# Kernel tuning notes

Measured on AMD Instinct MI355X. Metric: run time of the kernel, lower is better.

Reference implementation:

```python
import jax, jax.numpy as jnp
import numpy as np

DIM = 1024
N_HEADS = 16
B, S = 2, 2048


def setup_inputs() -> dict:
    key = jax.random.key(0)
    ks = jax.random.split(key, 9)
    scale = 1.0 / np.sqrt(DIM)
    return {
        "i1": jax.random.normal(ks[0], (B, S, DIM), jnp.float32),
        "i2": jax.random.normal(ks[1], (B, S, DIM), jnp.float32),
        "cr": jax.random.normal(ks[2], (B, S, 2), jnp.float32),
        # Linear params stored as [in, out] so forward is x @ W + b (same math as torch x W^T + b)
        "Wq": jax.random.normal(ks[3], (DIM, DIM), jnp.float32) * scale,
        "bq": jnp.zeros((DIM,), jnp.float32),
        "Wkv": jax.random.normal(ks[4], (DIM, 2 * DIM), jnp.float32) * scale,
        "bkv": jnp.zeros((2 * DIM,), jnp.float32),
        "Wmo": jax.random.normal(ks[5], (2, DIM), jnp.float32) * (1.0 / np.sqrt(2.0)),
        "bmo": jnp.zeros((DIM,), jnp.float32),
    }


def reference(i1, i2, cr, Wq, bq, Wkv, bkv, Wmo, bmo):
    H = N_HEADS
    Dh = DIM // H
    b, s, _ = i1.shape

    q = (i1 @ Wq + bq).reshape(b, s, H, Dh)                # [B,S,H,Dh]
    kv = i2 @ Wkv + bkv                                     # [B,S,2*DIM]
    k = kv[..., :DIM].reshape(b, s, H, Dh)
    v = kv[..., DIM:].reshape(b, s, H, Dh)
    mo = (cr @ Wmo + bmo).reshape(b, s, H, Dh)              # [B,S,H,Dh]

    scores = jnp.einsum("bqhd,bkhd->bhqk", q, k) / jnp.sqrt(jnp.asarray(Dh, q.dtype))
    probs = jax.nn.softmax(scores, axis=-1)                 # [B,H,S,S] (dropout p=0)

    h = jnp.einsum("bhqk,bkhd->bqhd", probs, v).reshape(b, s, DIM)
    m = jnp.einsum("bhqk,bkhd->bqhd", probs, mo).reshape(b, s, DIM)
    return h, m
```

## Files before the change

kernel.cpp:

```cpp
#include <hip/hip_runtime.h>
#include <hip/hip_bf16.h>

typedef __attribute__((ext_vector_type(8))) short short8;
typedef __attribute__((ext_vector_type(4))) short short4_t;
typedef __attribute__((ext_vector_type(4))) float f32x4;
typedef unsigned short ushort_t;

#define DEV __device__ __forceinline__

DEV ushort_t f2bf(float f) {
    unsigned u = __builtin_bit_cast(unsigned, f);
    u = u + 0x7fffu + ((u >> 16) & 1u);
    return (ushort_t)(u >> 16);
}

DEV unsigned pk_bf16(float lo, float hi) {
    __hip_bfloat162 h = __float22bfloat162_rn(make_float2(lo, hi));
    unsigned u;
    __builtin_memcpy(&u, &h, sizeof(u));
    return u;
}

DEV float fast_exp2(float x) {
#if __has_builtin(__builtin_amdgcn_exp2f)
    return __builtin_amdgcn_exp2f(x);
#else
    float r;
    asm("v_exp_f32 %0, %1" : "=v"(r) : "v"(x));
    return r;
#endif
}

DEV short8 ld8(const ushort_t* p) { return *reinterpret_cast<const short8*>(p); }

__global__ __launch_bounds__(256)
void cvt_bf16(const float* __restrict__ in, ushort_t* __restrict__ out)
{
    const size_t i = ((size_t)blockIdx.x * 256 + threadIdx.x) * 8;
    const float4 a = *reinterpret_cast<const float4*>(in + i);
    const float4 b = *reinterpret_cast<const float4*>(in + i + 4);
    short8 v;
    v[0] = (short)f2bf(a.x); v[1] = (short)f2bf(a.y);
    v[2] = (short)f2bf(a.z); v[3] = (short)f2bf(a.w);
    v[4] = (short)f2bf(b.x); v[5] = (short)f2bf(b.y);
    v[6] = (short)f2bf(b.z); v[7] = (short)f2bf(b.w);
    *reinterpret_cast<short8*>(out + i) = v;
}

__global__ __launch_bounds__(256)
void tcvt_bf16(const float* __restrict__ W, ushort_t* __restrict__ Wt, int K, int N)
{
    __shared__ ushort_t tile[64][72];
    const int t = threadIdx.x;
    const int nx = blockIdx.x * 64, ky = blockIdx.y * 64;
    const int r = t >> 2, q = (t & 3) * 16;

    const float* src = W + (size_t)(ky + r) * N + nx + q;
#pragma unroll
    for (int i = 0; i < 4; ++i) {
        const float4 v = *reinterpret_cast<const float4*>(src + 4 * i);
        tile[r][q + 4 * i + 0] = f2bf(v.x);
        tile[r][q + 4 * i + 1] = f2bf(v.y);
        tile[r][q + 4 * i + 2] = f2bf(v.z);
        tile[r][q + 4 * i + 3] = f2bf(v.w);
    }
    __syncthreads();
    short8 o0, o1;
#pragma unroll
    for (int i = 0; i < 8; ++i) {
        o0[i] = (short)tile[q + i][r];
        o1[i] = (short)tile[q + 8 + i][r];
    }
    ushort_t* dst = Wt + (size_t)(nx + r) * K + ky + q;
    *reinterpret_cast<short8*>(dst) = o0;
    *reinterpret_cast<short8*>(dst + 8) = o1;
}

__global__ __launch_bounds__(256, 2)
void proj_all(const ushort_t* __restrict__ A1, const ushort_t* __restrict__ A2,
              const ushort_t* __restrict__ Wqt, const ushort_t* __restrict__ Wkvt,
              const float* __restrict__ bqv, const float* __restrict__ bkv,
              ushort_t* __restrict__ Qr, ushort_t* __restrict__ Kr,
              ushort_t* __restrict__ Vt)
{
    __shared__ ushort_t As[128 * 72];
    __shared__ ushort_t Bs[128 * 72];

    const int t = threadIdx.x;
    const int lane = t & 63;
    const int wv = t >> 6;
    const int wr = wv >> 1, wc = wv & 1;
    const int c = lane & 15, g = lane >> 4;
    const int m0 = blockIdx.y * 128;
    const int nblk = blockIdx.x;

    const ushort_t* A;
    const ushort_t* Wt;
    const float* bias;
    int n0;
    if (nblk < 8) { A = A1; Wt = Wqt;  bias = bqv; n0 = nblk * 128; }
    else          { A = A2; Wt = Wkvt; bias = bkv; n0 = (nblk - 8) * 128; }
    const bool isQ = (nblk < 8);

    f32x4 acc[4][4];
    const f32x4 zero4 = {0.f, 0.f, 0.f, 0.f};
#pragma unroll
    for (int mi = 0; mi < 4; ++mi)
#pragma unroll
        for (int ni = 0; ni < 4; ++ni) acc[mi][ni] = zero4;

    const int srow[4] = { (t + 0)   >> 3, (t + 256) >> 3, (t + 512) >> 3, (t + 768) >> 3 };
    const int skq     = (t & 7) * 8;

    short8 a_reg[4], b_reg[4];
#pragma unroll
    for (int rep = 0; rep < 4; ++rep) {
        a_reg[rep] = ld8(A  + (size_t)(m0 + srow[rep]) * 1024 + skq);
        b_reg[rep] = ld8(Wt + (size_t)(n0 + srow[rep]) * 1024 + skq);
    }

    for (int it = 0; it < 16; ++it) {
#pragma unroll
        for (int rep = 0; rep < 4; ++rep) {
            *reinterpret_cast<short8*>(&As[srow[rep] * 72 + skq]) = a_reg[rep];
            *reinterpret_cast<short8*>(&Bs[srow[rep] * 72 + skq]) = b_reg[rep];
        }
        __syncthreads();
        if (it < 15) {
            const int k1 = (it + 1) * 64;
#pragma unroll
            for (int rep = 0; rep < 4; ++rep) {
                a_reg[rep] = ld8(A  + (size_t)(m0 + srow[rep]) * 1024 + k1 + skq);
                b_reg[rep] = ld8(Wt + (size_t)(n0 + srow[rep]) * 1024 + k1 + skq);
            }
        }
#pragma unroll
        for (int kk = 0; kk < 64; kk += 32) {
            short8 afr[4], bfr[4];
#pragma unroll
            for (int mi = 0; mi < 4; ++mi)
                afr[mi] = ld8(&As[(wr * 64 + mi * 16 + c) * 72 + kk + 8 * g]);
#pragma unroll
            for (int ni = 0; ni < 4; ++ni)
                bfr[ni] = ld8(&Bs[(wc * 64 + ni * 16 + c) * 72 + kk + 8 * g]);
#pragma unroll
            for (int mi = 0; mi < 4; ++mi)
#pragma unroll
                for (int ni = 0; ni < 4; ++ni)
                    acc[mi][ni] = __builtin_amdgcn_mfma_f32_16x16x32_bf16(
                        afr[mi], bfr[ni], acc[mi][ni], 0, 0, 0);
        }
        __syncthreads();
    }

#pragma unroll
    for (int mi = 0; mi < 4; ++mi) {
#pragma unroll
        for (int ni = 0; ni < 4; ++ni) {
            const int n = n0 + wc * 64 + ni * 16 + c;
            const float bb = bias[n];
#pragma unroll
            for (int j = 0; j < 4; ++j) {
                const int m = m0 + wr * 64 + mi * 16 + 4 * g + j;
                const int b = m >> 11, s = m & 2047;
                const ushort_t val = f2bf(acc[mi][ni][j] + bb);
                if (isQ) {
                    Qr[((size_t)((b * 16 + (n >> 6)) * 2048 + s)) * 64 + (n & 63)] = val;
                } else if (n < 1024) {
                    Kr[((size_t)((b * 16 + (n >> 6)) * 2048 + s)) * 64 + (n & 63)] = val;
                } else {
                    const int np = n - 1024;
                    Vt[(size_t)((b * 16 + (np >> 6)) * 64 + (np & 63)) * 2048 + s] = val;
                }
            }
        }
    }
}

__global__ __launch_bounds__(256)
void proj_gemm(const float* __restrict__ A, const float* __restrict__ W,
               const float* __restrict__ bias, int N,
               ushort_t* __restrict__ outRow, ushort_t* __restrict__ outT)
{
    __shared__ ushort_t As[128 * 72];
    __shared__ ushort_t Bt[128 * 72];

    const int t = threadIdx.x;
    const int lane = t & 63;
    const int wv = t >> 6;
    const int wr = wv >> 1, wc = wv & 1;
    const int c = lane & 15, g = lane >> 4;
    const int m0 = blockIdx.y * 128, n0 = blockIdx.x * 128;

    f32x4 acc[4][4];
    const f32x4 zero4 = {0.f, 0.f, 0.f, 0.f};
#pragma unroll
    for (int mi = 0; mi < 4; ++mi)
#pragma unroll
        for (int ni = 0; ni < 4; ++ni) acc[mi][ni] = zero4;

    for (int it = 0; it < 16; ++it) {
        const int k0 = it * 64;
        {
            const int kq = (t & 15) * 4;
            int r = t >> 4;
#pragma unroll
            for (int rep = 0; rep < 8; ++rep, r += 16) {
                float4 v = *reinterpret_cast<const float4*>(
                    A + (size_t)(m0 + r) * 1024 + k0 + kq);
                ushort_t* dst = &As[r * 72 + kq];
                dst[0] = f2bf(v.x); dst[1] = f2bf(v.y);
                dst[2] = f2bf(v.z); dst[3] = f2bf(v.w);
            }
        }
        {
            const int nq = (t & 31) * 4;
            const int kr = t >> 5;
#pragma unroll
            for (int rep = 0; rep < 8; ++rep) {
                const int k = kr + 8 * rep;
                float4 v = *reinterpret_cast<const float4*>(
                    W + (size_t)(k0 + k) * N + n0 + nq);
                Bt[(nq + 0) * 72 + k] = f2bf(v.x);
                Bt[(nq + 1) * 72 + k] = f2bf(v.y);
                Bt[(nq + 2) * 72 + k] = f2bf(v.z);
                Bt[(nq + 3) * 72 + k] = f2bf(v.w);
            }
        }
        __syncthreads();
#pragma unroll
        for (int kk = 0; kk < 64; kk += 32) {
            short8 afr[4], bfr[4];
#pragma unroll
            for (int mi = 0; mi < 4; ++mi)
                afr[mi] = ld8(&As[(wr * 64 + mi * 16 + c) * 72 + kk + 8 * g]);
#pragma unroll
            for (int ni = 0; ni < 4; ++ni)
                bfr[ni] = ld8(&Bt[(wc * 64 + ni * 16 + c) * 72 + kk + 8 * g]);
#pragma unroll
            for (int mi = 0; mi < 4; ++mi)
#pragma unroll
                for (int ni = 0; ni < 4; ++ni)
                    acc[mi][ni] = __builtin_amdgcn_mfma_f32_16x16x32_bf16(
                        afr[mi], bfr[ni], acc[mi][ni], 0, 0, 0);
        }
        __syncthreads();
    }

#pragma unroll
    for (int mi = 0; mi < 4; ++mi) {
#pragma unroll
        for (int ni = 0; ni < 4; ++ni) {
            const int n = n0 + wc * 64 + ni * 16 + c;
            const float bb = bias[n];
#pragma unroll
            for (int j = 0; j < 4; ++j) {
                const int m = m0 + wr * 64 + mi * 16 + 4 * g + j;
                const int b = m >> 11, s = m & 2047;
                const ushort_t val = f2bf(acc[mi][ni][j] + bb);
                if (outT != nullptr && n >= 1024) {
                    const int np = n - 1024;
                    const int hh = np >> 6, d = np & 63;
                    outT[(size_t)((b * 16 + hh) * 64 + d) * 2048 + s] = val;
                } else {
                    const int hh = n >> 6, d = n & 63;
                    outRow[((size_t)((b * 16 + hh) * 2048 + s)) * 64 + d] = val;
                }
            }
        }
    }
}

DEV void tile_compute(const ushort_t* __restrict__ Ks, const ushort_t* __restrict__ Vs,
                      const float* __restrict__ Crs, int c, int g,
                      const short8 (&bq)[2][2],
                      f32x4 (&accv)[2][4], float (&lst)[2],
                      float (&a0s)[2], float (&a1s)[2])
{
    const f32x4 zero4 = {0.f, 0.f, 0.f, 0.f};
    const float SCL = 0.18033688011112042f;
    const int kxor = (c & 7) << 3;
    const int vxor = (c & 7) << 2;

    short8 KC[2][2];
#pragma unroll
    for (int ct = 0; ct < 2; ++ct)
#pragma unroll
        for (int st = 0; st < 2; ++st)
            KC[ct][st] = ld8(&Ks[(ct * 16 + c) * 64 + ((st * 32 + 8 * g) ^ kxor)]);
    short8 VC[4];
#pragma unroll
    for (int dt = 0; dt < 4; ++dt) {
        const short4_t vlo = *reinterpret_cast<const short4_t*>(
            &Vs[(dt * 16 + c) * 32 + ((4 * g) ^ vxor)]);
        const short4_t vhi = *reinterpret_cast<const short4_t*>(
            &Vs[(dt * 16 + c) * 32 + ((4 * g + 16) ^ vxor)]);
        VC[dt] = __builtin_shufflevector(vlo, vhi, 0, 1, 2, 3, 4, 5, 6, 7);
    }
    float4 cc[2][2];
#pragma unroll
    for (int ct = 0; ct < 2; ++ct) {
        const float4* cp = reinterpret_cast<const float4*>(Crs + (16 * ct + 4 * g) * 2);
        cc[ct][0] = cp[0];
        cc[ct][1] = cp[1];
    }

    f32x4 sc[2][2];
#pragma unroll
    for (int qt = 0; qt < 2; ++qt)
#pragma unroll
        for (int ct = 0; ct < 2; ++ct) {
            f32x4 z = zero4;
            z = __builtin_amdgcn_mfma_f32_16x16x32_bf16(KC[ct][0], bq[qt][0], z, 0, 0, 0);
            z = __builtin_amdgcn_mfma_f32_16x16x32_bf16(KC[ct][1], bq[qt][1], z, 0, 0, 0);
            sc[qt][ct] = z;
        }

    short8 pa[2];
#pragma unroll
    for (int qt = 0; qt < 2; ++qt) {
        float e[2][4];
        float lc = lst[qt], a0c = a0s[qt], a1c = a1s[qt];
#pragma unroll
        for (int ct = 0; ct < 2; ++ct) {
            const float cr0[4] = {cc[ct][0].x, cc[ct][0].z, cc[ct][1].x, cc[ct][1].z};
            const float cr1[4] = {cc[ct][0].y, cc[ct][0].w, cc[ct][1].y, cc[ct][1].w};
#pragma unroll
            for (int j = 0; j < 4; ++j) {
                const float ev = fast_exp2(sc[qt][ct][j] * SCL);
                e[ct][j] = ev;
                lc  += ev;
                a0c += ev * cr0[j];
                a1c += ev * cr1[j];
            }
        }
        lst[qt] = lc; a0s[qt] = a0c; a1s[qt] = a1c;
        int4 w;
        w.x = (int)pk_bf16(e[0][0], e[0][1]);
        w.y = (int)pk_bf16(e[0][2], e[0][3]);
        w.z = (int)pk_bf16(e[1][0], e[1][1]);
        w.w = (int)pk_bf16(e[1][2], e[1][3]);
        pa[qt] = __builtin_bit_cast(short8, w);
    }

#pragma unroll
    for (int dt = 0; dt < 4; ++dt) {
        accv[0][dt] = __builtin_amdgcn_mfma_f32_16x16x32_bf16(VC[dt], pa[0], accv[0][dt], 0, 0, 0);
        accv[1][dt] = __builtin_amdgcn_mfma_f32_16x16x32_bf16(VC[dt], pa[1], accv[1][dt], 0, 0, 0);
    }
}

DEV void pair_body(const ushort_t* __restrict__ Kh, const ushort_t* __restrict__ Vh,
                   const float* __restrict__ crb, int kvA, int kvB,
                   const ushort_t* KsC0, const ushort_t* VsC0, const float* CrC0,
                   const ushort_t* KsC1, const ushort_t* VsC1, const float* CrC1,
                   ushort_t* KsN0, ushort_t* VsN0, float* CrN0,
                   ushort_t* KsN1, ushort_t* VsN1, float* CrN1,
                   int t, int c, int g, int rk, int ck, int rv, int cv,
                   int kaddr, int vaddr0, int vaddr1,
                   const short8 (&bq)[2][2],
                   f32x4 (&accv)[2][4], float (&lst)[2],
                   float (&a0s)[2], float (&a1s)[2])
{
    const short8 kregA = ld8(Kh + (size_t)(kvA + rk) * 64 + ck);
    const short8 vregA = ld8(Vh + (size_t)rv * 2048 + kvA + cv);
    const short8 kregB = ld8(Kh + (size_t)(kvB + rk) * 64 + ck);
    const short8 vregB = ld8(Vh + (size_t)rv * 2048 + kvB + cv);
    float2 crreg = make_float2(0.f, 0.f);
    if (t < 64) {
        const int kvX = (t & 32) ? kvB : kvA;
        crreg = *reinterpret_cast<const float2*>(crb + (size_t)(kvX + (t & 31)) * 2);
    }
    __builtin_amdgcn_sched_barrier(0);

    tile_compute(KsC0, VsC0, CrC0, c, g, bq, accv, lst, a0s, a1s);
    tile_compute(KsC1, VsC1, CrC1, c, g, bq, accv, lst, a0s, a1s);

    *reinterpret_cast<short8*>(&KsN0[kaddr]) = kregA;
    *reinterpret_cast<short8*>(&KsN1[kaddr]) = kregB;
    *reinterpret_cast<short4_t*>(&VsN0[vaddr0]) = __builtin_shufflevector(vregA, vregA, 0, 1, 2, 3);
    *reinterpret_cast<short4_t*>(&VsN0[vaddr1]) = __builtin_shufflevector(vregA, vregA, 4, 5, 6, 7);
    *reinterpret_cast<short4_t*>(&VsN1[vaddr0]) = __builtin_shufflevector(vregB, vregB, 0, 1, 2, 3);
    *reinterpret_cast<short4_t*>(&VsN1[vaddr1]) = __builtin_shufflevector(vregB, vregB, 4, 5, 6, 7);
    if (t < 64) {
        float* d = (t & 32) ? CrN1 : CrN0;
        *reinterpret_cast<float2*>(d + (t & 31) * 2) = crreg;
    }
    __syncthreads();
}

__global__ __launch_bounds__(256, 2)
void attn_kernel(const ushort_t* __restrict__ Qr, const ushort_t* __restrict__ Kr,
                 const ushort_t* __restrict__ Vt, const float* __restrict__ cr,
                 const float* __restrict__ Wmo, const float* __restrict__ bmo,
                 float* __restrict__ out)
{
    __shared__ ushort_t smem[16896];
    ushort_t* K0 = smem;            ushort_t* K1 = smem + 2048;
    ushort_t* K2 = smem + 4096;     ushort_t* K3 = smem + 6144;
    ushort_t* V0 = smem + 8192;     ushort_t* V1 = smem + 10240;
    ushort_t* V2 = smem + 12288;    ushort_t* V3 = smem + 14336;
    float* C0 = reinterpret_cast<float*>(smem + 16384);
    float* C1 = C0 + 64;  float* C2 = C0 + 128;  float* C3 = C0 + 192;

    const int t = threadIdx.x;
    const int w = t >> 6, lane = t & 63;
    const int c = lane & 15, g = lane >> 4;
    const int rk = t >> 3, ck = (t & 7) * 8;
    const int rv = t >> 2, cv = (t & 3) * 8;
    const int kaddr  = rk * 64 + (ck ^ ((rk & 7) << 3));
    const int vaddr0 = rv * 32 + (cv ^ ((rv & 7) << 2));
    const int vaddr1 = rv * 32 + ((cv + 4) ^ ((rv & 7) << 2));

    const int gid = blockIdx.x;
    const int bh = (gid & 7) + 8 * ((gid >> 3) & 3);
    const int xt = gid >> 5;
    const int b = bh >> 4, hh = bh & 15;
    const int qb = xt * 128 + w * 32;

    const ushort_t* Qh = Qr + (size_t)bh * (2048 * 64);
    const ushort_t* Kh = Kr + (size_t)bh * (2048 * 64);
    const ushort_t* Vh = Vt + (size_t)bh * (64 * 2048);
    const float*   crb = cr + (size_t)b * (2048 * 2);

    short8 bq[2][2];
#pragma unroll
    for (int qt = 0; qt < 2; ++qt)
#pragma unroll
        for (int st = 0; st < 2; ++st)
            bq[qt][st] = ld8(Qh + (size_t)(qb + qt * 16 + c) * 64 + st * 32 + 8 * g);

    f32x4 accv[2][4];
    const f32x4 zero4 = {0.f, 0.f, 0.f, 0.f};
#pragma unroll
    for (int qt = 0; qt < 2; ++qt)
#pragma unroll
        for (int dt = 0; dt < 4; ++dt) accv[qt][dt] = zero4;

    float lst[2] = {0.f, 0.f};
    float a0s[2] = {0.f, 0.f};
    float a1s[2] = {0.f, 0.f};

    {
        const short8 kA = ld8(Kh + (size_t)rk * 64 + ck);
        const short8 vA = ld8(Vh + (size_t)rv * 2048 + cv);
        const short8 kB = ld8(Kh + (size_t)(32 + rk) * 64 + ck);
        const short8 vB = ld8(Vh + (size_t)rv * 2048 + 32 + cv);
        *reinterpret_cast<short8*>(&K0[kaddr]) = kA;
        *reinterpret_cast<short8*>(&K1[kaddr]) = kB;
        *reinterpret_cast<short4_t*>(&V0[vaddr0]) = __builtin_shufflevector(vA, vA, 0, 1, 2, 3);
        *reinterpret_cast<short4_t*>(&V0[vaddr1]) = __builtin_shufflevector(vA, vA, 4, 5, 6, 7);
        *reinterpret_cast<short4_t*>(&V1[vaddr0]) = __builtin_shufflevector(vB, vB, 0, 1, 2, 3);
        *reinterpret_cast<short4_t*>(&V1[vaddr1]) = __builtin_shufflevector(vB, vB, 4, 5, 6, 7);
        if (t < 64) {
            const int kvX = (t & 32) ? 32 : 0;
            const float2 v = *reinterpret_cast<const float2*>(crb + (size_t)(kvX + (t & 31)) * 2);
            float* d = (t & 32) ? C1 : C0;
            *reinterpret_cast<float2*>(d + (t & 31) * 2) = v;
        }
    }
    __syncthreads();

    for (int i = 0; i < 16; ++i) {
        const int base = i * 128;
        pair_body(Kh, Vh, crb, base + 64, base + 96,
                  K0, V0, C0, K1, V1, C1,
                  K2, V2, C2, K3, V3, C3,
                  t, c, g, rk, ck, rv, cv, kaddr, vaddr0, vaddr1,
                  bq, accv, lst, a0s, a1s);
        pair_body(Kh, Vh, crb, (base + 128) & 2047, (base + 160) & 2047,
                  K2, V2, C2, K3, V3, C3,
                  K0, V0, C0, K1, V1, C1,
                  t, c, g, rk, ck, rv, cv, kaddr, vaddr0, vaddr1,
                  bq, accv, lst, a0s, a1s);
    }

#pragma unroll
    for (int qt = 0; qt < 2; ++qt) {
        lst[qt] += __shfl_xor(lst[qt], 16, 64); lst[qt] += __shfl_xor(lst[qt], 32, 64);
        a0s[qt] += __shfl_xor(a0s[qt], 16, 64); a0s[qt] += __shfl_xor(a0s[qt], 32, 64);
        a1s[qt] += __shfl_xor(a1s[qt], 16, 64); a1s[qt] += __shfl_xor(a1s[qt], 32, 64);
    }

#pragma unroll
    for (int qt = 0; qt < 2; ++qt) {
        const int q = qb + qt * 16 + c;
        const float inv = 1.f / lst[qt];
        const float a0 = a0s[qt] * inv, a1 = a1s[qt] * inv;
#pragma unroll
        for (int dt = 0; dt < 4; ++dt) {
            const int d = hh * 64 + dt * 16 + 4 * g;
            const float4 w0 = *reinterpret_cast<const float4*>(Wmo + d);
            const float4 w1 = *reinterpret_cast<const float4*>(Wmo + 1024 + d);
            const float4 bm = *reinterpret_cast<const float4*>(bmo + d);
            const size_t oidx = ((size_t)(b * 2048 + q)) * 1024 + d;
            float4 hv, mv;
            hv.x = accv[qt][dt][0] * inv; hv.y = accv[qt][dt][1] * inv;
            hv.z = accv[qt][dt][2] * inv; hv.w = accv[qt][dt][3] * inv;
            mv.x = a0 * w0.x + a1 * w1.x + bm.x;
            mv.y = a0 * w0.y + a1 * w1.y + bm.y;
            mv.z = a0 * w0.z + a1 * w1.z + bm.z;
            mv.w = a0 * w0.w + a1 * w1.w + bm.w;
            *reinterpret_cast<float4*>(out + oidx) = hv;
            *reinterpret_cast<float4*>(out + 4194304 + oidx) = mv;
        }
    }
}

extern "C" void kernel_launch(void* const* d_in, const int* in_sizes, int n_in,
                              void* d_out, int out_size, void* d_ws, size_t ws_size,
                              hipStream_t stream)
{
    const float* i1  = (const float*)d_in[0];
    const float* i2  = (const float*)d_in[1];
    const float* cr  = (const float*)d_in[2];
    const float* Wq  = (const float*)d_in[3];
    const float* bq  = (const float*)d_in[4];
    const float* Wkv = (const float*)d_in[5];
    const float* bkv = (const float*)d_in[6];
    const float* Wmo = (const float*)d_in[7];
    const float* bmo = (const float*)d_in[8];
    float* out = (float*)d_out;

    ushort_t* Qr = (ushort_t*)d_ws;
    ushort_t* Kr = Qr + 4194304;
    ushort_t* Vt = Kr + 4194304;

    if (ws_size >= 48234496ULL) {
        ushort_t* A1   = Vt + 4194304;
        ushort_t* A2   = A1 + 4194304;
        ushort_t* Wqt  = A2 + 4194304;
        ushort_t* Wkvt = Wqt + 1048576;
        cvt_bf16<<<dim3(2048), dim3(256), 0, stream>>>(i1, A1);
        cvt_bf16<<<dim3(2048), dim3(256), 0, stream>>>(i2, A2);
        tcvt_bf16<<<dim3(16, 16), dim3(256), 0, stream>>>(Wq, Wqt, 1024, 1024);
        tcvt_bf16<<<dim3(32, 16), dim3(256), 0, stream>>>(Wkv, Wkvt, 1024, 2048);
        proj_all<<<dim3(24, 32), dim3(256), 0, stream>>>(A1, A2, Wqt, Wkvt, bq, bkv, Qr, Kr, Vt);
    } else {
        proj_gemm<<<dim3(8, 32), dim3(256), 0, stream>>>(i1, Wq, bq, 1024, Qr, nullptr);
        proj_gemm<<<dim3(16, 32), dim3(256), 0, stream>>>(i2, Wkv, bkv, 2048, Kr, Vt);
    }
    attn_kernel<<<dim3(512), dim3(256), 0, stream>>>(Qr, Kr, Vt, cr, Wmo, bmo, out);
}
```

Before: 122.2 us.

## Compute softmax row-sum and cr moments via MFMA, fold scale into Q projection

The per-element VALU accumulation of the softmax denominator and the two cr-weighted sums is replaced by an extra MFMA per q-tile. It multiplies a small bf16 stats tile (a row of ones, two rows of cr values, zero padding) against the probability fragments. The softmax scale is also folded into the Q projection epilogue, which removes a multiply before each exp2. This moves VALU work onto the matrix cores, at the cost of bf16 rounding of cr values and of Q after scaling, plus a little extra shared memory.

```diff
diff --git a/kernel.cpp b/kernel.cpp
--- a/kernel.cpp
+++ b/kernel.cpp
@@ -32,6 +32,8 @@
 }
 
 DEV short8 ld8(const ushort_t* p) { return *reinterpret_cast<const short8*>(p); }
+
+#define SCL_F 0.18033688011112042f
 
 __global__ __launch_bounds__(256)
 void cvt_bf16(const float* __restrict__ in, ushort_t* __restrict__ out)
@@ -101,6 +103,7 @@
     if (nblk < 8) { A = A1; Wt = Wqt;  bias = bqv; n0 = nblk * 128; }
     else          { A = A2; Wt = Wkvt; bias = bkv; n0 = (nblk - 8) * 128; }
     const bool isQ = (nblk < 8);
+    const float qscale = isQ ? SCL_F : 1.0f;
 
     f32x4 acc[4][4];
     const f32x4 zero4 = {0.f, 0.f, 0.f, 0.f};
@@ -163,7 +166,7 @@
             for (int j = 0; j < 4; ++j) {
                 const int m = m0 + wr * 64 + mi * 16 + 4 * g + j;
                 const int b = m >> 11, s = m & 2047;
-                const ushort_t val = f2bf(acc[mi][ni][j] + bb);
+                const ushort_t val = f2bf((acc[mi][ni][j] + bb) * qscale);
                 if (isQ) {
                     Qr[((size_t)((b * 16 + (n >> 6)) * 2048 + s)) * 64 + (n & 63)] = val;
                 } else if (n < 1024) {
@@ -191,6 +194,7 @@
     const int wr = wv >> 1, wc = wv & 1;
     const int c = lane & 15, g = lane >> 4;
     const int m0 = blockIdx.y * 128, n0 = blockIdx.x * 128;
+    const float qscale = (outT == nullptr) ? SCL_F : 1.0f;
 
     f32x4 acc[4][4];
     const f32x4 zero4 = {0.f, 0.f, 0.f, 0.f};
@@ -257,7 +261,7 @@
             for (int j = 0; j < 4; ++j) {
                 const int m = m0 + wr * 64 + mi * 16 + 4 * g + j;
                 const int b = m >> 11, s = m & 2047;
-                const ushort_t val = f2bf(acc[mi][ni][j] + bb);
+                const ushort_t val = f2bf((acc[mi][ni][j] + bb) * qscale);
                 if (outT != nullptr && n >= 1024) {
                     const int np = n - 1024;
                     const int hh = np >> 6, d = np & 63;
@@ -272,13 +276,11 @@
 }
 
 DEV void tile_compute(const ushort_t* __restrict__ Ks, const ushort_t* __restrict__ Vs,
-                      const float* __restrict__ Crs, int c, int g,
+                      const ushort_t* __restrict__ Sts, int c, int g,
                       const short8 (&bq)[2][2],
-                      f32x4 (&accv)[2][4], float (&lst)[2],
-                      float (&a0s)[2], float (&a1s)[2])
+                      f32x4 (&accv)[2][4], f32x4 (&stat)[2])
 {
     const f32x4 zero4 = {0.f, 0.f, 0.f, 0.f};
-    const float SCL = 0.18033688011112042f;
     const int kxor = (c & 7) << 3;
     const int vxor = (c & 7) << 2;
 
@@ -297,13 +299,11 @@
             &Vs[(dt * 16 + c) * 32 + ((4 * g + 16) ^ vxor)]);
         VC[dt] = __builtin_shufflevector(vlo, vhi, 0, 1, 2, 3, 4, 5, 6, 7);
     }
-    float4 cc[2][2];
-#pragma unroll
-    for (int ct = 0; ct < 2; ++ct) {
-        const float4* cp = reinterpret_cast<const float4*>(Crs + (16 * ct + 4 * g) * 2);
-        cc[ct][0] = cp[0];
-        cc[ct][1] = cp[1];
-    }
+    const short4_t slo = *reinterpret_cast<const short4_t*>(
+        &Sts[c * 32 + ((4 * g) ^ vxor)]);
+    const short4_t shi = *reinterpret_cast<const short4_t*>(
+        &Sts[c * 32 + ((4 * g + 16) ^ vxor)]);
+    const short8 stf = __builtin_shufflevector(slo, shi, 0, 1, 2, 3, 4, 5, 6, 7);
 
     f32x4 sc[2][2];
 #pragma unroll
@@ -320,21 +320,11 @@
 #pragma unroll
     for (int qt = 0; qt < 2; ++qt) {
         float e[2][4];
-        float lc = lst[qt], a0c = a0s[qt], a1c = a1s[qt];
-#pragma unroll
-        for (int ct = 0; ct < 2; ++ct) {
-            const float cr0[4] = {cc[ct][0].x, cc[ct][0].z, cc[ct][1].x, cc[ct][1].z};
-            const float cr1[4] = {cc[ct][0].y, cc[ct][0].w, cc[ct][1].y, cc[ct][1].w};
-#pragma unroll
-            for (int j = 0; j < 4; ++j) {
-                const float ev = fast_exp2(sc[qt][ct][j] * SCL);
-                e[ct][j] = ev;
-                lc  += ev;
-                a0c += ev * cr0[j];
-                a1c += ev * cr1[j];
-            }
-        }
-        lst[qt] = lc; a0s[qt] = a0c; a1s[qt] = a1c;
+#pragma unroll
+        for (int ct = 0; ct < 2; ++ct)
+#pragma unroll
+            for (int j = 0; j < 4; ++j)
+                e[ct][j] = fast_exp2(sc[qt][ct][j]);
         int4 w;
         w.x = (int)pk_bf16(e[0][0], e[0][1]);
         w.y = (int)pk_bf16(e[0][2], e[0][3]);
@@ -344,6 +334,9 @@
     }
 
 #pragma unroll
+    for (int qt = 0; qt < 2; ++qt)
+        stat[qt] = __builtin_amdgcn_mfma_f32_16x16x32_bf16(stf, pa[qt], stat[qt], 0, 0, 0);
+#pragma unroll
     for (int dt = 0; dt < 4; ++dt) {
         accv[0][dt] = __builtin_amdgcn_mfma_f32_16x16x32_bf16(VC[dt], pa[0], accv[0][dt], 0, 0, 0);
         accv[1][dt] = __builtin_amdgcn_mfma_f32_16x16x32_bf16(VC[dt], pa[1], accv[1][dt], 0, 0, 0);
@@ -352,29 +345,31 @@
 
 DEV void pair_body(const ushort_t* __restrict__ Kh, const ushort_t* __restrict__ Vh,
                    const float* __restrict__ crb, int kvA, int kvB,
-                   const ushort_t* KsC0, const ushort_t* VsC0, const float* CrC0,
-                   const ushort_t* KsC1, const ushort_t* VsC1, const float* CrC1,
-                   ushort_t* KsN0, ushort_t* VsN0, float* CrN0,
-                   ushort_t* KsN1, ushort_t* VsN1, float* CrN1,
+                   const ushort_t* KsC0, const ushort_t* VsC0, const ushort_t* StC0,
+                   const ushort_t* KsC1, const ushort_t* VsC1, const ushort_t* StC1,
+                   ushort_t* KsN0, ushort_t* VsN0, ushort_t* StN0,
+                   ushort_t* KsN1, ushort_t* VsN1, ushort_t* StN1,
                    int t, int c, int g, int rk, int ck, int rv, int cv,
                    int kaddr, int vaddr0, int vaddr1,
                    const short8 (&bq)[2][2],
-                   f32x4 (&accv)[2][4], float (&lst)[2],
-                   float (&a0s)[2], float (&a1s)[2])
+                   f32x4 (&accv)[2][4], f32x4 (&stat)[2])
 {
     const short8 kregA = ld8(Kh + (size_t)(kvA + rk) * 64 + ck);
     const short8 vregA = ld8(Vh + (size_t)rv * 2048 + kvA + cv);
     const short8 kregB = ld8(Kh + (size_t)(kvB + rk) * 64 + ck);
     const short8 vregB = ld8(Vh + (size_t)rv * 2048 + kvB + cv);
-    float2 crreg = make_float2(0.f, 0.f);
-    if (t < 64) {
-        const int kvX = (t & 32) ? kvB : kvA;
-        crreg = *reinterpret_cast<const float2*>(crb + (size_t)(kvX + (t & 31)) * 2);
+    ushort_t crsh = 0; int staddr = 0;
+    if (t < 128) {
+        const int kvX = (t & 64) ? kvB : kvA;
+        const int row = 1 + ((t >> 5) & 1);
+        const float v = crb[(size_t)(kvX + (t & 31)) * 2 + (row - 1)];
+        crsh = f2bf(v);
+        staddr = row * 32 + ((t & 31) ^ ((row & 7) << 2));
     }
     __builtin_amdgcn_sched_barrier(0);
 
-    tile_compute(KsC0, VsC0, CrC0, c, g, bq, accv, lst, a0s, a1s);
-    tile_compute(KsC1, VsC1, CrC1, c, g, bq, accv, lst, a0s, a1s);
+    tile_compute(KsC0, VsC0, StC0, c, g, bq, accv, stat);
+    tile_compute(KsC1, VsC1, StC1, c, g, bq, accv, stat);
 
     *reinterpret_cast<short8*>(&KsN0[kaddr]) = kregA;
     *reinterpret_cast<short8*>(&KsN1[kaddr]) = kregB;
@@ -382,10 +377,7 @@
     *reinterpret_cast<short4_t*>(&VsN0[vaddr1]) = __builtin_shufflevector(vregA, vregA, 4, 5, 6, 7);
     *reinterpret_cast<short4_t*>(&VsN1[vaddr0]) = __builtin_shufflevector(vregB, vregB, 0, 1, 2, 3);
     *reinterpret_cast<short4_t*>(&VsN1[vaddr1]) = __builtin_shufflevector(vregB, vregB, 4, 5, 6, 7);
-    if (t < 64) {
-        float* d = (t & 32) ? CrN1 : CrN0;
-        *reinterpret_cast<float2*>(d + (t & 31) * 2) = crreg;
-    }
+    if (t < 128) ((t & 64) ? StN1 : StN0)[staddr] = crsh;
     __syncthreads();
 }
 
@@ -395,13 +387,13 @@
                  const float* __restrict__ Wmo, const float* __restrict__ bmo,
                  float* __restrict__ out)
 {
-    __shared__ ushort_t smem[16896];
+    __shared__ ushort_t smem[18432];
     ushort_t* K0 = smem;            ushort_t* K1 = smem + 2048;
     ushort_t* K2 = smem + 4096;     ushort_t* K3 = smem + 6144;
     ushort_t* V0 = smem + 8192;     ushort_t* V1 = smem + 10240;
     ushort_t* V2 = smem + 12288;    ushort_t* V3 = smem + 14336;
-    float* C0 = reinterpret_cast<float*>(smem + 16384);
-    float* C1 = C0 + 64;  float* C2 = C0 + 128;  float* C3 = C0 + 192;
+    ushort_t* S0 = smem + 16384;    ushort_t* S1 = smem + 16896;
+    ushort_t* S2 = smem + 17408;    ushort_t* S3 = smem + 17920;
 
     const int t = threadIdx.x;
     const int w = t >> 6, lane = t & 63;
@@ -431,15 +423,20 @@
             bq[qt][st] = ld8(Qh + (size_t)(qb + qt * 16 + c) * 64 + st * 32 + 8 * g);
 
     f32x4 accv[2][4];
+    f32x4 stat[2];
     const f32x4 zero4 = {0.f, 0.f, 0.f, 0.f};
 #pragma unroll
-    for (int qt = 0; qt < 2; ++qt)
+    for (int qt = 0; qt < 2; ++qt) {
+        stat[qt] = zero4;
 #pragma unroll
         for (int dt = 0; dt < 4; ++dt) accv[qt][dt] = zero4;
-
-    float lst[2] = {0.f, 0.f};
-    float a0s[2] = {0.f, 0.f};
-    float a1s[2] = {0.f, 0.f};
+    }
+
+    for (int idx = t; idx < 2048; idx += 256) {
+        const int row = (idx >> 5) & 15;
+        if (row != 1 && row != 2)
+            smem[16384 + idx] = (row == 0) ? (ushort_t)0x3F80 : (ushort_t)0;
+    }
 
     {
         const short8 kA = ld8(Kh + (size_t)rk * 64 + ck);
@@ -452,11 +449,11 @@
         *reinterpret_cast<short4_t*>(&V0[vaddr1]) = __builtin_shufflevector(vA, vA, 4, 5, 6, 7);
         *reinterpret_cast<short4_t*>(&V1[vaddr0]) = __builtin_shufflevector(vB, vB, 0, 1, 2, 3);
         *reinterpret_cast<short4_t*>(&V1[vaddr1]) = __builtin_shufflevector(vB, vB, 4, 5, 6, 7);
-        if (t < 64) {
-            const int kvX = (t & 32) ? 32 : 0;
-            const float2 v = *reinterpret_cast<const float2*>(crb + (size_t)(kvX + (t & 31)) * 2);
-            float* d = (t & 32) ? C1 : C0;
-            *reinterpret_cast<float2*>(d + (t & 31) * 2) = v;
+        if (t < 128) {
+            const int kvX = (t & 64) ? 32 : 0;
+            const int row = 1 + ((t >> 5) & 1);
+            const float v = crb[(size_t)(kvX + (t & 31)) * 2 + (row - 1)];
+            ((t & 64) ? S1 : S0)[row * 32 + ((t & 31) ^ ((row & 7) << 2))] = f2bf(v);
         }
     }
     __syncthreads();
@@ -464,22 +461,23 @@
     for (int i = 0; i < 16; ++i) {
         const int base = i * 128;
         pair_body(Kh, Vh, crb, base + 64, base + 96,
-                  K0, V0, C0, K1, V1, C1,
-                  K2, V2, C2, K3, V3, C3,
+                  K0, V0, S0, K1, V1, S1,
+                  K2, V2, S2, K3, V3, S3,
                   t, c, g, rk, ck, rv, cv, kaddr, vaddr0, vaddr1,
-                  bq, accv, lst, a0s, a1s);
+                  bq, accv, stat);
         pair_body(Kh, Vh, crb, (base + 128) & 2047, (base + 160) & 2047,
-                  K2, V2, C2, K3, V3, C3,
-                  K0, V0, C0, K1, V1, C1,
+                  K2, V2, S2, K3, V3, S3,
+                  K0, V0, S0, K1, V1, S1,
                   t, c, g, rk, ck, rv, cv, kaddr, vaddr0, vaddr1,
-                  bq, accv, lst, a0s, a1s);
-    }
-
+                  bq, accv, stat);
+    }
+
+    float lst[2], a0s[2], a1s[2];
 #pragma unroll
     for (int qt = 0; qt < 2; ++qt) {
-        lst[qt] += __shfl_xor(lst[qt], 16, 64); lst[qt] += __shfl_xor(lst[qt], 32, 64);
-        a0s[qt] += __shfl_xor(a0s[qt], 16, 64); a0s[qt] += __shfl_xor(a0s[qt], 32, 64);
-        a1s[qt] += __shfl_xor(a1s[qt], 16, 64); a1s[qt] += __shfl_xor(a1s[qt], 32, 64);
+        lst[qt] = __shfl(stat[qt][0], c, 64);
+        a0s[qt] = __shfl(stat[qt][1], c, 64);
+        a1s[qt] = __shfl(stat[qt][2], c, 64);
     }
 
 #pragma unroll
```

Measured after the change: 115.7 us. -5.3%, faster.
